# Kernel tuning notes

Measured on AMD Instinct MI355X. Metric: run time of the kernel, lower is better.

## Reference

```python
import jax, jax.numpy as jnp
import numpy as np
import math

HIDDEN = 128; NHEADS = 4; N_COE = 50; N_SCALES = 4; THRE = 5.0; S = 4096; B = 1


def setup_inputs():
    key = jax.random.key(0)
    ks = jax.random.split(key, 12)
    w = lambda k, shape: jax.random.normal(k, shape, jnp.float32) * 0.05
    return {
        "eigenvalue": jax.random.uniform(ks[0], (B, S), jnp.float32) * 2.0,  # graph Laplacian eigvals in [0,2)
        "length": jnp.full((B,), S, dtype=jnp.int32),
        "sele_num": jnp.full((B,), S, dtype=jnp.int32),
        "eig_w_W": w(ks[1], (HIDDEN + 1, HIDDEN)), "eig_w_b": jnp.zeros((HIDDEN,), jnp.float32),
        "mha_ln_g": jnp.ones((HIDDEN,), jnp.float32), "mha_ln_b": jnp.zeros((HIDDEN,), jnp.float32),
        "in_W": w(ks[2], (HIDDEN, 3 * HIDDEN)), "in_b": jnp.zeros((3 * HIDDEN,), jnp.float32),
        "out_W": w(ks[3], (HIDDEN, HIDDEN)), "out_b": jnp.zeros((HIDDEN,), jnp.float32),
        "ffn_ln_g": jnp.ones((HIDDEN,), jnp.float32), "ffn_ln_b": jnp.zeros((HIDDEN,), jnp.float32),
        "ffn1_W": w(ks[4], (HIDDEN, HIDDEN)), "ffn1_b": jnp.zeros((HIDDEN,), jnp.float32),
        "ffn2_W": w(ks[5], (HIDDEN, HIDDEN)), "ffn2_b": jnp.zeros((HIDDEN,), jnp.float32),
        "dsc_W": w(ks[6], (HIDDEN, N_COE)), "dsc_b": jnp.zeros((N_COE,), jnp.float32),
        "dwv_W": w(ks[7], (HIDDEN, N_COE)), "dwv_b": jnp.zeros((N_COE,), jnp.float32),
        "dss_W": w(ks[8], (HIDDEN, N_SCALES)), "dss_b": jnp.zeros((N_SCALES,), jnp.float32),
    }


def layer_norm(x, g, b, eps=1e-5):
    m = x.mean(-1, keepdims=True)
    v = ((x - m) ** 2).mean(-1, keepdims=True)
    return (x - m) / jnp.sqrt(v + eps) * g + b


def sine_encoding(e, W, b):
    # e: [B, S] -> [B, S, HIDDEN]
    div = jnp.exp(jnp.arange(0, HIDDEN, 2, dtype=e.dtype) * (-math.log(10000.0) / HIDDEN))
    pe = (e * 100.0)[..., None] * div  # [B, S, HIDDEN/2]
    eeig = jnp.concatenate([e[..., None], jnp.sin(pe), jnp.cos(pe)], axis=-1)  # [B, S, HIDDEN+1]
    return eeig @ W + b


def mha(x, pad_mask, in_W, in_b, out_W, out_b):
    # x: [B, S, D]; pad_mask: [B, S] True = masked key
    Bb, Ss, D = x.shape
    hd = D // NHEADS
    qkv = x @ in_W + in_b
    q, k, v = jnp.split(qkv, 3, axis=-1)
    hsplit = lambda t: t.reshape(Bb, Ss, NHEADS, hd).transpose(0, 2, 1, 3)  # [B, H, S, hd]
    q, k, v = hsplit(q), hsplit(k), hsplit(v)
    scores = jnp.einsum('bhqd,bhkd->bhqk', q, k) / math.sqrt(hd)
    scores = jnp.where(pad_mask[:, None, None, :], -jnp.inf, scores)
    attn = jax.nn.softmax(scores, axis=-1)
    o = jnp.einsum('bhqk,bhkd->bhqd', attn, v).transpose(0, 2, 1, 3).reshape(Bb, Ss, D)
    return o @ out_W + out_b


def cheb_base(y, n_coe, flag):
    # Chebyshev recurrence: wavelet = [T_0, T_2, ...], scaling = [T_1, T_3, ...]
    te0 = jnp.ones_like(y)
    to0 = y
    def step(carry, _):
        te, to = carry
        te = 2.0 * y * to - te
        to = 2.0 * y * te - to
        return (te, to), (te, to)
    _, (evens, odds) = jax.lax.scan(step, (te0, to0), None, length=n_coe - 1)
    if flag == 'scaling':
        base = jnp.concatenate([to0[None], odds], axis=0)   # [n_coe, B, S, d]
    else:
        base = jnp.concatenate([te0[None], evens], axis=0)
    return jnp.moveaxis(base, 0, 1)  # [B, n_coe, S, d]


def _forward(eigenvalue, eig_w_W, eig_w_b, mha_ln_g, mha_ln_b, in_W, in_b, out_W, out_b,
             ffn_ln_g, ffn_ln_b, ffn1_W, ffn1_b, ffn2_W, ffn2_b,
             dsc_W, dsc_b, dwv_W, dwv_b, dss_W, dss_b, length, sele_num):
    Bb, Ss = eigenvalue.shape
    eve = eigenvalue
    eig_mask = jnp.arange(Ss)[None, :] >= sele_num[:, None]  # [B, S] True = pad
    # --- EigenEncoding (dropout in eval mode = identity) ---
    eig = sine_encoding(eve, eig_w_W, eig_w_b)
    eig = eig + mha(layer_norm(eig, mha_ln_g, mha_ln_b), eig_mask, in_W, in_b, out_W, out_b)
    f = layer_norm(eig, ffn_ln_g, ffn_ln_b)
    f = jax.nn.gelu(f @ ffn1_W + ffn1_b, approximate=False) @ ffn2_W + ffn2_b
    eig_filter = eig + f  # [B, S, HIDDEN]
    lenf = length.astype(eve.dtype)[:, None]
    def pooled(W, b):
        c = eig_filter @ W + b
        c = jnp.where(eig_mask[..., None], 0.0, c)
        return c.sum(axis=1) / (lenf + 1e-8)
    coe_scaling = jax.nn.sigmoid(pooled(dsc_W, dsc_b))
    coe_scaling = coe_scaling / (coe_scaling.sum(-1, keepdims=True) + 1e-8)  # [B, n_coe]
    coe_wavelet = jax.nn.sigmoid(pooled(dwv_W, dwv_b))
    coe_wavelet = coe_wavelet / (coe_wavelet.sum(-1, keepdims=True) + 1e-8)
    coe_scales = jax.nn.sigmoid(pooled(dss_W, dss_b)) * THRE  # [B, n_scales]
    # --- Chebyshev bases ---
    base_scaling = cheb_base(eve[..., None] - 1.0, N_COE, 'scaling')  # [B, n_coe, S, 1]
    fsw = eve[..., None] * coe_scales[:, None, :]                      # [B, S, n_scales]
    fsw = jnp.where(fsw > 2.0, 0.0, fsw)
    base_wavelet = cheb_base(fsw - 1.0, N_COE, 'wavelet')             # [B, n_coe, S, n_scales]
    base_scaling = 0.5 * (1.0 - base_scaling)
    base_wavelet = 0.5 * (1.0 - base_wavelet)
    curr_scaling = jnp.einsum('bc,bcsd->bsd', coe_scaling, base_scaling)
    curr_wavelet = jnp.einsum('bc,bcsd->bsd', coe_wavelet, base_wavelet)
    out = jnp.concatenate([curr_scaling, curr_wavelet], axis=-1)       # [B, S, 1+n_scales]
    out = out / (jnp.linalg.norm(out, axis=-1, keepdims=True) + 1e-8)  # cfg.lam.tight_use = True
    return out


def reference(eigenvalue, length, sele_num, eig_w_W, eig_w_b, mha_ln_g, mha_ln_b, in_W, in_b,
              out_W, out_b, ffn_ln_g, ffn_ln_b, ffn1_W, ffn1_b, ffn2_W, ffn2_b,
              dsc_W, dsc_b, dwv_W, dwv_b, dss_W, dss_b):
    return _forward(eigenvalue, eig_w_W, eig_w_b, mha_ln_g, mha_ln_b, in_W, in_b, out_W, out_b,
                    ffn_ln_g, ffn_ln_b, ffn1_W, ffn1_b, ffn2_W, ffn2_b,
                    dsc_W, dsc_b, dwv_W, dwv_b, dss_W, dss_b, length, sele_num)
```

## Files before the change

kernel.cpp:

```cpp
#include <hip/hip_runtime.h>
#include <math.h>


#define KSPLIT 4

typedef __attribute__((ext_vector_type(8))) short short8;
typedef __attribute__((ext_vector_type(4))) short short4v;
typedef __attribute__((ext_vector_type(4))) float f32x4;

__device__ inline unsigned short f2bf(float x) {
    unsigned u = __float_as_uint(x);
    return (unsigned short)((u + 0x7FFFu + ((u >> 16) & 1u)) >> 16);
}
__device__ inline float bf2f(unsigned short h) { return __uint_as_float(((unsigned)h) << 16); }

__global__ __launch_bounds__(256) void k_embed(const float* __restrict__ eve,
    const float* __restrict__ eigW, const float* __restrict__ ebias,
    const float* __restrict__ g, const float* __restrict__ b,
    const float* __restrict__ inW, const float* __restrict__ inb,
    float* __restrict__ eig, float* __restrict__ qkv, unsigned short* __restrict__ Khi_g,
    unsigned short* __restrict__ Klo_g, unsigned short* __restrict__ Vt_g)
{
    __shared__ __align__(16) float wsh[129 * 128];
    __shared__ __align__(16) float se[16][132];
    __shared__ __align__(16) float xn[16][132];
    __shared__ __align__(16) unsigned short vsh[128][16];
    const int t = threadIdx.x;
    const int r0 = blockIdx.x * 16;
    {
        const int r = t >> 4, l4 = t & 15;
        const float e = eve[r0 + r];
        if (l4 == 0) se[r][128] = e;
        #pragma unroll
        for (int jj = 0; jj < 4; ++jj) {
            const int j = l4 * 4 + jj;
            const float div = __expf(-0.07195578415606394f * (float)(2 * j));
            const float pe = e * 100.0f * div;
            se[r][j]      = __sinf(pe);
            se[r][64 + j] = __cosf(pe);
        }
    }
    {
        const float4* __restrict__ src = (const float4*)eigW;
        float4* dst = (float4*)wsh;
        #pragma unroll
        for (int i = 0; i < 17; ++i) {
            const int f = t + i * 256;
            if (f < 4128) dst[f] = src[f];
        }
    }
    __syncthreads();
    const int lane = t & 63;
    const int w = t >> 6;
    const int rp = w * 2 + (lane >> 5);
    const int c0 = (lane & 31) * 4;
    const int ra = rp * 2, rb = ra + 1;
    float xa[4], xb[4];
    {
        const float4 w0 = *(const float4*)&wsh[c0];
        const float ea = se[ra][128], eb = se[rb][128];
        float a0 = ea * w0.x, a1 = ea * w0.y, a2 = ea * w0.z, a3 = ea * w0.w;
        float b0 = eb * w0.x, b1 = eb * w0.y, b2 = eb * w0.z, b3 = eb * w0.w;
        #pragma unroll 8
        for (int k = 0; k < 128; ++k) {
            const float xva = se[ra][k];
            const float xvb = se[rb][k];
            const float4 wk = *(const float4*)&wsh[(k + 1) * 128 + c0];
            a0 = fmaf(xva, wk.x, a0); a1 = fmaf(xva, wk.y, a1);
            a2 = fmaf(xva, wk.z, a2); a3 = fmaf(xva, wk.w, a3);
            b0 = fmaf(xvb, wk.x, b0); b1 = fmaf(xvb, wk.y, b1);
            b2 = fmaf(xvb, wk.z, b2); b3 = fmaf(xvb, wk.w, b3);
        }
        const float4 bb = *(const float4*)&ebias[c0];
        xa[0] = a0 + bb.x; xa[1] = a1 + bb.y; xa[2] = a2 + bb.z; xa[3] = a3 + bb.w;
        xb[0] = b0 + bb.x; xb[1] = b1 + bb.y; xb[2] = b2 + bb.z; xb[3] = b3 + bb.w;
        *(float4*)&eig[(size_t)(r0 + ra) * 128 + c0] = make_float4(xa[0], xa[1], xa[2], xa[3]);
        *(float4*)&eig[(size_t)(r0 + rb) * 128 + c0] = make_float4(xb[0], xb[1], xb[2], xb[3]);
    }
    {
        float sa = (xa[0] + xa[1]) + (xa[2] + xa[3]);
        float qa = (xa[0] * xa[0] + xa[1] * xa[1]) + (xa[2] * xa[2] + xa[3] * xa[3]);
        float sb = (xb[0] + xb[1]) + (xb[2] + xb[3]);
        float qb = (xb[0] * xb[0] + xb[1] * xb[1]) + (xb[2] * xb[2] + xb[3] * xb[3]);
        #pragma unroll
        for (int m = 1; m < 32; m <<= 1) {
            sa += __shfl_xor(sa, m, 32); qa += __shfl_xor(qa, m, 32);
            sb += __shfl_xor(sb, m, 32); qb += __shfl_xor(qb, m, 32);
        }
        const float ma = sa * (1.f / 128.f), mb = sb * (1.f / 128.f);
        const float ia = 1.f / sqrtf(qa * (1.f / 128.f) - ma * ma + 1e-5f);
        const float ib = 1.f / sqrtf(qb * (1.f / 128.f) - mb * mb + 1e-5f);
        const float4 gg = *(const float4*)&g[c0];
        const float4 bb = *(const float4*)&b[c0];
        *(float4*)&xn[ra][c0] = make_float4((xa[0] - ma) * ia * gg.x + bb.x,
                                            (xa[1] - ma) * ia * gg.y + bb.y,
                                            (xa[2] - ma) * ia * gg.z + bb.z,
                                            (xa[3] - ma) * ia * gg.w + bb.w);
        *(float4*)&xn[rb][c0] = make_float4((xb[0] - mb) * ib * gg.x + bb.x,
                                            (xb[1] - mb) * ib * gg.y + bb.y,
                                            (xb[2] - mb) * ib * gg.z + bb.z,
                                            (xb[3] - mb) * ib * gg.w + bb.w);
    }
    const int rowa = r0 + ra, rowb = r0 + rb;
    for (int p = 0; p < 3; ++p) {
        __syncthreads();
        {
            const float4* __restrict__ src = (const float4*)inW;
            float4* dst = (float4*)wsh;
            #pragma unroll
            for (int i = 0; i < 16; ++i) {
                const int f = t + i * 256;
                const int k = f >> 5, c4 = f & 31;
                dst[f] = src[k * 96 + p * 32 + c4];
            }
        }
        __syncthreads();
        float A[4], B[4];
        {
            const float4 bb = *(const float4*)&inb[p * 128 + c0];
            A[0] = bb.x; A[1] = bb.y; A[2] = bb.z; A[3] = bb.w;
            B[0] = bb.x; B[1] = bb.y; B[2] = bb.z; B[3] = bb.w;
        }
        #pragma unroll 8
        for (int k = 0; k < 128; ++k) {
            const float xva = xn[ra][k];
            const float xvb = xn[rb][k];
            const float4 wk = *(const float4*)&wsh[k * 128 + c0];
            A[0] = fmaf(xva, wk.x, A[0]); A[1] = fmaf(xva, wk.y, A[1]);
            A[2] = fmaf(xva, wk.z, A[2]); A[3] = fmaf(xva, wk.w, A[3]);
            B[0] = fmaf(xvb, wk.x, B[0]); B[1] = fmaf(xvb, wk.y, B[1]);
            B[2] = fmaf(xvb, wk.z, B[2]); B[3] = fmaf(xvb, wk.w, B[3]);
        }
        if (p == 0) {
            *(float4*)&qkv[(size_t)rowa * 384 + c0] = make_float4(A[0], A[1], A[2], A[3]);
            *(float4*)&qkv[(size_t)rowb * 384 + c0] = make_float4(B[0], B[1], B[2], B[3]);
        } else if (p == 1) {
            const int h = c0 >> 5, d = c0 & 31;
            unsigned short h4[4], l4v[4];
            #pragma unroll
            for (int i = 0; i < 4; ++i) { h4[i] = f2bf(A[i]); l4v[i] = f2bf(A[i] - bf2f(h4[i])); }
            *(uint2*)&Khi_g[((size_t)h * 4096 + rowa) * 32 + d] = *(uint2*)h4;
            *(uint2*)&Klo_g[((size_t)h * 4096 + rowa) * 32 + d] = *(uint2*)l4v;
            #pragma unroll
            for (int i = 0; i < 4; ++i) { h4[i] = f2bf(B[i]); l4v[i] = f2bf(B[i] - bf2f(h4[i])); }
            *(uint2*)&Khi_g[((size_t)h * 4096 + rowb) * 32 + d] = *(uint2*)h4;
            *(uint2*)&Klo_g[((size_t)h * 4096 + rowb) * 32 + d] = *(uint2*)l4v;
        } else {
            #pragma unroll
            for (int i = 0; i < 4; ++i) {
                vsh[c0 + i][ra] = f2bf(A[i]);
                vsh[c0 + i][rb] = f2bf(B[i]);
            }
        }
    }
    __syncthreads();
    if (t < 128) {
        const uint4 v0 = *(const uint4*)&vsh[t][0];
        const uint4 v1 = *(const uint4*)&vsh[t][8];
        *(uint4*)&Vt_g[(size_t)t * 4096 + r0]     = v0;
        *(uint4*)&Vt_g[(size_t)t * 4096 + r0 + 8] = v1;
    }
}

#define KSTR 40
#define VSTR 72
#define PSTR 72

__global__ __launch_bounds__(256) void k_attn(const float* __restrict__ qkv,
    const unsigned short* __restrict__ Khi_g, const unsigned short* __restrict__ Klo_g,
    const unsigned short* __restrict__ Vt_g,
    const int* __restrict__ sele, float* __restrict__ Oe, float* __restrict__ E)
{
    __shared__ __align__(16) unsigned short Khi[64 * KSTR];
    __shared__ __align__(16) unsigned short Klo[64 * KSTR];
    __shared__ __align__(16) unsigned short Vt[32 * VSTR];
    __shared__ __align__(16) unsigned short Pb[4][16 * PSTR];

    const int t = threadIdx.x;
    const int lane = t & 63;
    const int l = lane & 15;
    const int quad = lane >> 4;
    const int wv = __builtin_amdgcn_readfirstlane(t >> 6);
    const int qb = blockIdx.x;
    const int h  = blockIdx.y;
    const int ks = blockIdx.z;
    const int nk = sele[0];

    short8 qhi, qlo;
    {
        const float* __restrict__ qr = qkv + (size_t)(qb * 64 + wv * 16 + l) * 384 + h * 32 + quad * 8;
        const float4 a = *(const float4*)qr;
        const float4 b = *(const float4*)(qr + 4);
        const float sc = 0.17677669529663687f;
        float v[8] = {a.x * sc, a.y * sc, a.z * sc, a.w * sc, b.x * sc, b.y * sc, b.z * sc, b.w * sc};
        #pragma unroll
        for (int j = 0; j < 8; ++j) {
            const unsigned short hb = f2bf(v[j]);
            qhi[j] = (short)hb;
            qlo[j] = (short)f2bf(v[j] - bf2f(hb));
        }
    }
    f32x4 accO0 = {0.f, 0.f, 0.f, 0.f};
    f32x4 accO1 = {0.f, 0.f, 0.f, 0.f};
    float elane = 0.f;

    const int kk = t >> 2;
    const int d0 = (t & 3) * 8;
    const int vd = t >> 3;
    const int ko = (t & 7) * 8;

    for (int ch = 0; ch < 16; ++ch) {
        const int keybase = ks * 1024 + ch * 64;
        __syncthreads();
        {
            const uint4 kh16 = *(const uint4*)&Khi_g[((size_t)h * 4096 + keybase + kk) * 32 + d0];
            const uint4 kl16 = *(const uint4*)&Klo_g[((size_t)h * 4096 + keybase + kk) * 32 + d0];
            const uint4 vv16 = *(const uint4*)&Vt_g[((size_t)h * 32 + vd) * 4096 + keybase + ko];
            *(uint4*)&Khi[kk * KSTR + d0] = kh16;
            *(uint4*)&Klo[kk * KSTR + d0] = kl16;
            *(uint4*)&Vt[vd * VSTR + ko]  = vv16;
        }
        __syncthreads();
        unsigned short* __restrict__ Pw = Pb[wv];
        #pragma unroll
        for (int tile = 0; tile < 4; ++tile) {
            const int kl = tile * 16 + l;
            const short8 kh = *(const short8*)&Khi[kl * KSTR + quad * 8];
            const short8 kw = *(const short8*)&Klo[kl * KSTR + quad * 8];
            f32x4 S = {0.f, 0.f, 0.f, 0.f};
            S = __builtin_amdgcn_mfma_f32_16x16x32_bf16(kh, qhi, S, 0, 0, 0);
            S = __builtin_amdgcn_mfma_f32_16x16x32_bf16(kw, qhi, S, 0, 0, 0);
            S = __builtin_amdgcn_mfma_f32_16x16x32_bf16(kh, qlo, S, 0, 0, 0);
            const int kg0 = keybase + tile * 16 + quad * 4;
            short4v pw;
            #pragma unroll
            for (int r = 0; r < 4; ++r) {
                const float p = (kg0 + r < nk) ? __expf(S[r]) : 0.f;
                elane += p;
                pw[r] = (short)f2bf(p);
            }
            *(short4v*)&Pw[l * PSTR + tile * 16 + quad * 4] = pw;
        }
        #pragma unroll
        for (int step = 0; step < 2; ++step) {
            const short8 pa  = *(const short8*)&Pw[l * PSTR + step * 32 + quad * 8];
            const short8 vb0 = *(const short8*)&Vt[l * VSTR + step * 32 + quad * 8];
            const short8 vb1 = *(const short8*)&Vt[(16 + l) * VSTR + step * 32 + quad * 8];
            accO0 = __builtin_amdgcn_mfma_f32_16x16x32_bf16(pa, vb0, accO0, 0, 0, 0);
            accO1 = __builtin_amdgcn_mfma_f32_16x16x32_bf16(pa, vb1, accO1, 0, 0, 0);
        }
    }
    elane += __shfl_xor(elane, 16, 64);
    elane += __shfl_xor(elane, 32, 64);
    const int qrow0 = qb * 64 + wv * 16;
    if (lane < 16)
        E[((size_t)ks * 4 + h) * 4096 + qrow0 + l] = elane;
    #pragma unroll
    for (int r = 0; r < 4; ++r) {
        const size_t row = qrow0 + quad * 4 + r;
        Oe[((size_t)ks * 4096 + row) * 128 + h * 32 + l]      = accO0[r];
        Oe[((size_t)ks * 4096 + row) * 128 + h * 32 + 16 + l] = accO1[r];
    }
}

__global__ __launch_bounds__(256) void k_ffn(const float* __restrict__ eig,
    const float* __restrict__ Oe, const float* __restrict__ E,
    const float* __restrict__ outW, const float* __restrict__ outb,
    const float* __restrict__ lg, const float* __restrict__ lb,
    const float* __restrict__ W1, const float* __restrict__ b1,
    const float* __restrict__ W2, const float* __restrict__ b2,
    const int* __restrict__ sele, float* __restrict__ xsum)
{
    __shared__ __align__(16) float wsh[128 * 128];
    __shared__ __align__(16) float sA[16][132];
    __shared__ __align__(16) float xn[16][132];
    __shared__ __align__(16) float cs[16][132];
    const int t = threadIdx.x;
    const int r0 = blockIdx.x * 16;
    {
        const int r = t >> 4, c8 = (t & 15) * 8;
        const int h = c8 >> 5;
        float es = 0.f;
        float v[8] = {0.f, 0.f, 0.f, 0.f, 0.f, 0.f, 0.f, 0.f};
        #pragma unroll
        for (int ks = 0; ks < KSPLIT; ++ks) {
            es += E[((size_t)ks * 4 + h) * 4096 + r0 + r];
            const float4 o1 = *(const float4*)&Oe[((size_t)ks * 4096 + r0 + r) * 128 + c8];
            const float4 o2 = *(const float4*)&Oe[((size_t)ks * 4096 + r0 + r) * 128 + c8 + 4];
            v[0] += o1.x; v[1] += o1.y; v[2] += o1.z; v[3] += o1.w;
            v[4] += o2.x; v[5] += o2.y; v[6] += o2.z; v[7] += o2.w;
        }
        const float rcp = 1.f / es;
        *(float4*)&sA[r][c8]     = make_float4(v[0] * rcp, v[1] * rcp, v[2] * rcp, v[3] * rcp);
        *(float4*)&sA[r][c8 + 4] = make_float4(v[4] * rcp, v[5] * rcp, v[6] * rcp, v[7] * rcp);
    }
    {
        const float4* __restrict__ src = (const float4*)outW;
        float4* dst = (float4*)wsh;
        #pragma unroll
        for (int i = 0; i < 16; ++i) dst[t + i * 256] = src[t + i * 256];
    }
    __syncthreads();
    const int lane = t & 63;
    const int w = t >> 6;
    const int rp = w * 2 + (lane >> 5);
    const int c0 = (lane & 31) * 4;
    const int ra = rp * 2, rb = ra + 1;
    float x2a[4], x2b[4];
    {
        const float4 bb = *(const float4*)&outb[c0];
        float a0 = bb.x, a1 = bb.y, a2 = bb.z, a3 = bb.w;
        float b0 = bb.x, b1 = bb.y, b2 = bb.z, b3 = bb.w;
        #pragma unroll 8
        for (int k = 0; k < 128; ++k) {
            const float xva = sA[ra][k];
            const float xvb = sA[rb][k];
            const float4 wk = *(const float4*)&wsh[k * 128 + c0];
            a0 = fmaf(xva, wk.x, a0); a1 = fmaf(xva, wk.y, a1);
            a2 = fmaf(xva, wk.z, a2); a3 = fmaf(xva, wk.w, a3);
            b0 = fmaf(xvb, wk.x, b0); b1 = fmaf(xvb, wk.y, b1);
            b2 = fmaf(xvb, wk.z, b2); b3 = fmaf(xvb, wk.w, b3);
        }
        const float4 ea = *(const float4*)&eig[(size_t)(r0 + ra) * 128 + c0];
        const float4 eb = *(const float4*)&eig[(size_t)(r0 + rb) * 128 + c0];
        x2a[0] = ea.x + a0; x2a[1] = ea.y + a1; x2a[2] = ea.z + a2; x2a[3] = ea.w + a3;
        x2b[0] = eb.x + b0; x2b[1] = eb.y + b1; x2b[2] = eb.z + b2; x2b[3] = eb.w + b3;
    }
    {
        float sa = (x2a[0] + x2a[1]) + (x2a[2] + x2a[3]);
        float qa = (x2a[0] * x2a[0] + x2a[1] * x2a[1]) + (x2a[2] * x2a[2] + x2a[3] * x2a[3]);
        float sb = (x2b[0] + x2b[1]) + (x2b[2] + x2b[3]);
        float qb = (x2b[0] * x2b[0] + x2b[1] * x2b[1]) + (x2b[2] * x2b[2] + x2b[3] * x2b[3]);
        #pragma unroll
        for (int m = 1; m < 32; m <<= 1) {
            sa += __shfl_xor(sa, m, 32); qa += __shfl_xor(qa, m, 32);
            sb += __shfl_xor(sb, m, 32); qb += __shfl_xor(qb, m, 32);
        }
        const float ma = sa * (1.f / 128.f), mb = sb * (1.f / 128.f);
        const float ia = 1.f / sqrtf(qa * (1.f / 128.f) - ma * ma + 1e-5f);
        const float ib = 1.f / sqrtf(qb * (1.f / 128.f) - mb * mb + 1e-5f);
        const float4 gg = *(const float4*)&lg[c0];
        const float4 bb = *(const float4*)&lb[c0];
        *(float4*)&xn[ra][c0] = make_float4((x2a[0] - ma) * ia * gg.x + bb.x,
                                            (x2a[1] - ma) * ia * gg.y + bb.y,
                                            (x2a[2] - ma) * ia * gg.z + bb.z,
                                            (x2a[3] - ma) * ia * gg.w + bb.w);
        *(float4*)&xn[rb][c0] = make_float4((x2b[0] - mb) * ib * gg.x + bb.x,
                                            (x2b[1] - mb) * ib * gg.y + bb.y,
                                            (x2b[2] - mb) * ib * gg.z + bb.z,
                                            (x2b[3] - mb) * ib * gg.w + bb.w);
    }
    __syncthreads();
    {
        const float4* __restrict__ src = (const float4*)W1;
        float4* dst = (float4*)wsh;
        #pragma unroll
        for (int i = 0; i < 16; ++i) dst[t + i * 256] = src[t + i * 256];
    }
    __syncthreads();
    {
        const float4 bb = *(const float4*)&b1[c0];
        float a0 = bb.x, a1 = bb.y, a2 = bb.z, a3 = bb.w;
        float b0 = bb.x, b1v = bb.y, b2v = bb.z, b3 = bb.w;
        #pragma unroll 8
        for (int k = 0; k < 128; ++k) {
            const float xva = xn[ra][k];
            const float xvb = xn[rb][k];
            const float4 wk = *(const float4*)&wsh[k * 128 + c0];
            a0 = fmaf(xva, wk.x, a0); a1 = fmaf(xva, wk.y, a1);
            a2 = fmaf(xva, wk.z, a2); a3 = fmaf(xva, wk.w, a3);
            b0 = fmaf(xvb, wk.x, b0); b1v = fmaf(xvb, wk.y, b1v);
            b2v = fmaf(xvb, wk.z, b2v); b3 = fmaf(xvb, wk.w, b3);
        }
        *(float4*)&sA[ra][c0] = make_float4(
            0.5f * a0 * (1.f + erff(a0 * 0.70710678118654752f)),
            0.5f * a1 * (1.f + erff(a1 * 0.70710678118654752f)),
            0.5f * a2 * (1.f + erff(a2 * 0.70710678118654752f)),
            0.5f * a3 * (1.f + erff(a3 * 0.70710678118654752f)));
        *(float4*)&sA[rb][c0] = make_float4(
            0.5f * b0 * (1.f + erff(b0 * 0.70710678118654752f)),
            0.5f * b1v * (1.f + erff(b1v * 0.70710678118654752f)),
            0.5f * b2v * (1.f + erff(b2v * 0.70710678118654752f)),
            0.5f * b3 * (1.f + erff(b3 * 0.70710678118654752f)));
    }
    __syncthreads();
    {
        const float4* __restrict__ src = (const float4*)W2;
        float4* dst = (float4*)wsh;
        #pragma unroll
        for (int i = 0; i < 16; ++i) dst[t + i * 256] = src[t + i * 256];
    }
    __syncthreads();
    {
        const float4 bb = *(const float4*)&b2[c0];
        float a0 = bb.x, a1 = bb.y, a2 = bb.z, a3 = bb.w;
        float b0 = bb.x, b1v = bb.y, b2v = bb.z, b3 = bb.w;
        #pragma unroll 8
        for (int k = 0; k < 128; ++k) {
            const float xva = sA[ra][k];
            const float xvb = sA[rb][k];
            const float4 wk = *(const float4*)&wsh[k * 128 + c0];
            a0 = fmaf(xva, wk.x, a0); a1 = fmaf(xva, wk.y, a1);
            a2 = fmaf(xva, wk.z, a2); a3 = fmaf(xva, wk.w, a3);
            b0 = fmaf(xvb, wk.x, b0); b1v = fmaf(xvb, wk.y, b1v);
            b2v = fmaf(xvb, wk.z, b2v); b3 = fmaf(xvb, wk.w, b3);
        }
        const int nsel = sele[0];
        const bool ina = (r0 + ra) < nsel, inb2 = (r0 + rb) < nsel;
        *(float4*)&cs[ra][c0] = ina ? make_float4(x2a[0] + a0, x2a[1] + a1, x2a[2] + a2, x2a[3] + a3)
                                    : make_float4(0.f, 0.f, 0.f, 0.f);
        *(float4*)&cs[rb][c0] = inb2 ? make_float4(x2b[0] + b0, x2b[1] + b1v, x2b[2] + b2v, x2b[3] + b3)
                                     : make_float4(0.f, 0.f, 0.f, 0.f);
    }
    __syncthreads();
    if (t < 128) {
        float s = 0.f;
        #pragma unroll
        for (int rr = 0; rr < 16; ++rr) s += cs[rr][t];
        atomicAdd(&xsum[t], s);
    }
}

__global__ __launch_bounds__(512) void k_coef(const float* __restrict__ xsum,
    const float* __restrict__ dscW, const float* __restrict__ dscb,
    const float* __restrict__ dwvW, const float* __restrict__ dwvb,
    const float* __restrict__ dssW, const float* __restrict__ dssb,
    const int* __restrict__ len, const int* __restrict__ sele,
    float* __restrict__ coef)
{
    __shared__ float xs[128];
    __shared__ float part[104][4];
    __shared__ float val[104];
    __shared__ float s2[2];
    const int t = threadIdx.x;
    if (t < 128) xs[t] = xsum[t];
    __syncthreads();
    const float invl = 1.f / ((float)len[0] + 1e-8f);
    const float ns = (float)sele[0];
    const int o = t >> 2, lk = t & 3;
    if (o < 104) {
        const float* Wp; int stride, col;
        if (o < 50)       { Wp = dscW; stride = 50; col = o; }
        else if (o < 100) { Wp = dwvW; stride = 50; col = o - 50; }
        else              { Wp = dssW; stride = 4;  col = o - 100; }
        float a = 0.f;
        #pragma unroll
        for (int kk = 0; kk < 32; ++kk) {
            const int k = lk * 32 + kk;
            a = fmaf(xs[k], Wp[k * stride + col], a);
        }
        part[o][lk] = a;
    }
    __syncthreads();
    if (t < 104) {
        const float bias = (t < 50) ? dscb[t] : ((t < 100) ? dwvb[t - 50] : dssb[t - 100]);
        float a = ((part[t][0] + part[t][1]) + (part[t][2] + part[t][3]) + ns * bias) * invl;
        val[t] = 1.f / (1.f + __expf(-a));
    }
    __syncthreads();
    if (t == 0) { float s = 0.f; for (int i = 0; i < 50; ++i) s += val[i]; s2[0] = s; }
    if (t == 1) { float s = 0.f; for (int i = 0; i < 50; ++i) s += val[50 + i]; s2[1] = s; }
    __syncthreads();
    if (t < 50) {
        coef[t]      = val[t] / (s2[0] + 1e-8f);
        coef[50 + t] = val[50 + t] / (s2[1] + 1e-8f);
    } else if (t >= 100 && t < 104) {
        coef[t] = val[t] * 5.0f;
    }
}

__global__ __launch_bounds__(128) void k_out(const float* __restrict__ eve,
    const float* __restrict__ coef, float* __restrict__ out)
{
    __shared__ float csc[50], cwv[50], cssh[4];
    const int t = threadIdx.x;
    if (t < 50) csc[t] = coef[t];
    else if (t < 100) cwv[t - 50] = coef[t];
    else if (t < 104) cssh[t - 100] = coef[t];
    __syncthreads();
    const int s = blockIdx.x * 128 + t;
    const float e = eve[s];
    float vals[5];
    {
        const float y = e - 1.f;
        float te = 1.f, to = y;
        float a = csc[0] * (0.5f * (1.f - to));
        const float y2 = 2.f * y;
        for (int i = 1; i < 50; ++i) {
            te = fmaf(y2, to, -te);
            to = fmaf(y2, te, -to);
            a = fmaf(csc[i], 0.5f * (1.f - to), a);
        }
        vals[0] = a;
    }
    #pragma unroll
    for (int j = 0; j < 4; ++j) {
        float f = e * cssh[j];
        if (f > 2.f) f = 0.f;
        const float y = f - 1.f;
        float te = 1.f, to = y;
        float a = cwv[0] * (0.5f * (1.f - te));
        const float y2 = 2.f * y;
        for (int i = 1; i < 50; ++i) {
            te = fmaf(y2, to, -te);
            to = fmaf(y2, te, -to);
            a = fmaf(cwv[i], 0.5f * (1.f - te), a);
        }
        vals[1 + j] = a;
    }
    float n2 = 0.f;
    #pragma unroll
    for (int k = 0; k < 5; ++k) n2 += vals[k] * vals[k];
    const float invn = 1.f / (sqrtf(n2) + 1e-8f);
    #pragma unroll
    for (int k = 0; k < 5; ++k) out[s * 5 + k] = vals[k] * invn;
}

extern "C" void kernel_launch(void* const* d_in, const int* in_sizes, int n_in,
                              void* d_out, int out_size, void* d_ws, size_t ws_size,
                              hipStream_t stream) {
    const float* eve  = (const float*)d_in[0];
    const int*   len  = (const int*)d_in[1];
    const int*   sele = (const int*)d_in[2];
    const float* eigW = (const float*)d_in[3];
    const float* eigB = (const float*)d_in[4];
    const float* mlg  = (const float*)d_in[5];
    const float* mlb  = (const float*)d_in[6];
    const float* inW  = (const float*)d_in[7];
    const float* inb  = (const float*)d_in[8];
    const float* outW = (const float*)d_in[9];
    const float* outb = (const float*)d_in[10];
    const float* flg  = (const float*)d_in[11];
    const float* flb  = (const float*)d_in[12];
    const float* W1   = (const float*)d_in[13];
    const float* b1   = (const float*)d_in[14];
    const float* W2   = (const float*)d_in[15];
    const float* b2   = (const float*)d_in[16];
    const float* dscW = (const float*)d_in[17];
    const float* dscb = (const float*)d_in[18];
    const float* dwvW = (const float*)d_in[19];
    const float* dwvb = (const float*)d_in[20];
    const float* dssW = (const float*)d_in[21];
    const float* dssb = (const float*)d_in[22];

    float* ws   = (float*)d_ws;
    float* eig  = ws;
    float* qkv  = ws + 524288;
    float* Oe   = ws + 2097152;
    float* E    = ws + 4194304;
    float* xsum = ws + 4259840;
    float* coef = ws + 4259968;
    unsigned short* Khi_g = (unsigned short*)(ws + 4260352);
    unsigned short* Klo_g = (unsigned short*)(ws + 4522496);
    unsigned short* Vt_g  = (unsigned short*)(ws + 4784640);
    float* out  = (float*)d_out;

    hipMemsetAsync(xsum, 0, 128 * sizeof(float), stream);
    k_embed<<<256, 256, 0, stream>>>(eve, eigW, eigB, mlg, mlb, inW, inb,
                                     eig, qkv, Khi_g, Klo_g, Vt_g);
    k_attn <<<dim3(64, 4, KSPLIT), 256, 0, stream>>>(qkv, Khi_g, Klo_g, Vt_g, sele, Oe, E);
    k_ffn  <<<256, 256, 0, stream>>>(eig, Oe, E, outW, outb, flg, flb, W1, b1, W2, b2, sele, xsum);
    k_coef <<<1, 512, 0, stream>>>(xsum, dscW, dscb, dwvW, dwvb, dssW, dssb, len, sele, coef);
    k_out  <<<32, 128, 0, stream>>>(eve, coef, out);
}
```

Measured before the change: 187.8 us.

## Fold xsum memset into embed, merge coef into output kernel, widen blocks

The memset of the feature-sum buffer moves into the first block of the embed kernel. The single-block coefficient kernel is merged into the output kernel, and each of the 32 blocks now recomputes the coefficients redundantly. The embed and FFN kernels move from 256 to 512 threads with one row per thread group instead of two, which doubles parallelism per block but halves register-level reuse of the LDS weight loads. The changes aim to remove two launches and the memset node, at the cost of redundant tail compute and possibly more LDS traffic.

```diff
diff --git a/kernel.cpp b/kernel.cpp
--- a/kernel.cpp
+++ b/kernel.cpp
@@ -14,26 +14,28 @@
 }
 __device__ inline float bf2f(unsigned short h) { return __uint_as_float(((unsigned)h) << 16); }
 
-__global__ __launch_bounds__(256) void k_embed(const float* __restrict__ eve,
+__global__ __launch_bounds__(512) void k_embed(const float* __restrict__ eve,
     const float* __restrict__ eigW, const float* __restrict__ ebias,
     const float* __restrict__ g, const float* __restrict__ b,
     const float* __restrict__ inW, const float* __restrict__ inb,
     float* __restrict__ eig, float* __restrict__ qkv, unsigned short* __restrict__ Khi_g,
-    unsigned short* __restrict__ Klo_g, unsigned short* __restrict__ Vt_g)
+    unsigned short* __restrict__ Klo_g, unsigned short* __restrict__ Vt_g,
+    float* __restrict__ xsum)
 {
     __shared__ __align__(16) float wsh[129 * 128];
     __shared__ __align__(16) float se[16][132];
     __shared__ __align__(16) float xn[16][132];
-    __shared__ __align__(16) unsigned short vsh[128][16];
+    __shared__ __align__(16) unsigned short vsh[16][136];
     const int t = threadIdx.x;
     const int r0 = blockIdx.x * 16;
-    {
-        const int r = t >> 4, l4 = t & 15;
+    if (blockIdx.x == 0 && t < 128) xsum[t] = 0.f;
+    {
+        const int r = t >> 5, l5 = t & 31;
         const float e = eve[r0 + r];
-        if (l4 == 0) se[r][128] = e;
-        #pragma unroll
-        for (int jj = 0; jj < 4; ++jj) {
-            const int j = l4 * 4 + jj;
+        if (l5 == 0) se[r][128] = e;
+        #pragma unroll
+        for (int jj = 0; jj < 2; ++jj) {
+            const int j = l5 * 2 + jj;
             const float div = __expf(-0.07195578415606394f * (float)(2 * j));
             const float pe = e * 100.0f * div;
             se[r][j]      = __sinf(pe);
@@ -44,121 +46,95 @@
         const float4* __restrict__ src = (const float4*)eigW;
         float4* dst = (float4*)wsh;
         #pragma unroll
-        for (int i = 0; i < 17; ++i) {
-            const int f = t + i * 256;
+        for (int i = 0; i < 9; ++i) {
+            const int f = t + i * 512;
             if (f < 4128) dst[f] = src[f];
         }
     }
     __syncthreads();
-    const int lane = t & 63;
-    const int w = t >> 6;
-    const int rp = w * 2 + (lane >> 5);
-    const int c0 = (lane & 31) * 4;
-    const int ra = rp * 2, rb = ra + 1;
-    float xa[4], xb[4];
+    const int r  = t >> 5;
+    const int c0 = (t & 31) * 4;
+    float xa[4];
     {
         const float4 w0 = *(const float4*)&wsh[c0];
-        const float ea = se[ra][128], eb = se[rb][128];
+        const float ea = se[r][128];
         float a0 = ea * w0.x, a1 = ea * w0.y, a2 = ea * w0.z, a3 = ea * w0.w;
-        float b0 = eb * w0.x, b1 = eb * w0.y, b2 = eb * w0.z, b3 = eb * w0.w;
         #pragma unroll 8
         for (int k = 0; k < 128; ++k) {
-            const float xva = se[ra][k];
-            const float xvb = se[rb][k];
+            const float xv = se[r][k];
             const float4 wk = *(const float4*)&wsh[(k + 1) * 128 + c0];
-            a0 = fmaf(xva, wk.x, a0); a1 = fmaf(xva, wk.y, a1);
-            a2 = fmaf(xva, wk.z, a2); a3 = fmaf(xva, wk.w, a3);
-            b0 = fmaf(xvb, wk.x, b0); b1 = fmaf(xvb, wk.y, b1);
-            b2 = fmaf(xvb, wk.z, b2); b3 = fmaf(xvb, wk.w, b3);
+            a0 = fmaf(xv, wk.x, a0); a1 = fmaf(xv, wk.y, a1);
+            a2 = fmaf(xv, wk.z, a2); a3 = fmaf(xv, wk.w, a3);
         }
         const float4 bb = *(const float4*)&ebias[c0];
         xa[0] = a0 + bb.x; xa[1] = a1 + bb.y; xa[2] = a2 + bb.z; xa[3] = a3 + bb.w;
-        xb[0] = b0 + bb.x; xb[1] = b1 + bb.y; xb[2] = b2 + bb.z; xb[3] = b3 + bb.w;
-        *(float4*)&eig[(size_t)(r0 + ra) * 128 + c0] = make_float4(xa[0], xa[1], xa[2], xa[3]);
-        *(float4*)&eig[(size_t)(r0 + rb) * 128 + c0] = make_float4(xb[0], xb[1], xb[2], xb[3]);
+        *(float4*)&eig[(size_t)(r0 + r) * 128 + c0] = make_float4(xa[0], xa[1], xa[2], xa[3]);
     }
     {
         float sa = (xa[0] + xa[1]) + (xa[2] + xa[3]);
         float qa = (xa[0] * xa[0] + xa[1] * xa[1]) + (xa[2] * xa[2] + xa[3] * xa[3]);
-        float sb = (xb[0] + xb[1]) + (xb[2] + xb[3]);
-        float qb = (xb[0] * xb[0] + xb[1] * xb[1]) + (xb[2] * xb[2] + xb[3] * xb[3]);
         #pragma unroll
         for (int m = 1; m < 32; m <<= 1) {
             sa += __shfl_xor(sa, m, 32); qa += __shfl_xor(qa, m, 32);
-            sb += __shfl_xor(sb, m, 32); qb += __shfl_xor(qb, m, 32);
-        }
-        const float ma = sa * (1.f / 128.f), mb = sb * (1.f / 128.f);
+        }
+        const float ma = sa * (1.f / 128.f);
         const float ia = 1.f / sqrtf(qa * (1.f / 128.f) - ma * ma + 1e-5f);
-        const float ib = 1.f / sqrtf(qb * (1.f / 128.f) - mb * mb + 1e-5f);
         const float4 gg = *(const float4*)&g[c0];
         const float4 bb = *(const float4*)&b[c0];
-        *(float4*)&xn[ra][c0] = make_float4((xa[0] - ma) * ia * gg.x + bb.x,
-                                            (xa[1] - ma) * ia * gg.y + bb.y,
-                                            (xa[2] - ma) * ia * gg.z + bb.z,
-                                            (xa[3] - ma) * ia * gg.w + bb.w);
-        *(float4*)&xn[rb][c0] = make_float4((xb[0] - mb) * ib * gg.x + bb.x,
-                                            (xb[1] - mb) * ib * gg.y + bb.y,
-                                            (xb[2] - mb) * ib * gg.z + bb.z,
-                                            (xb[3] - mb) * ib * gg.w + bb.w);
-    }
-    const int rowa = r0 + ra, rowb = r0 + rb;
+        *(float4*)&xn[r][c0] = make_float4((xa[0] - ma) * ia * gg.x + bb.x,
+                                           (xa[1] - ma) * ia * gg.y + bb.y,
+                                           (xa[2] - ma) * ia * gg.z + bb.z,
+                                           (xa[3] - ma) * ia * gg.w + bb.w);
+    }
+    const int row = r0 + r;
     for (int p = 0; p < 3; ++p) {
         __syncthreads();
         {
             const float4* __restrict__ src = (const float4*)inW;
             float4* dst = (float4*)wsh;
             #pragma unroll
-            for (int i = 0; i < 16; ++i) {
-                const int f = t + i * 256;
+            for (int i = 0; i < 8; ++i) {
+                const int f = t + i * 512;
                 const int k = f >> 5, c4 = f & 31;
                 dst[f] = src[k * 96 + p * 32 + c4];
             }
         }
         __syncthreads();
-        float A[4], B[4];
+        float A[4];
         {
             const float4 bb = *(const float4*)&inb[p * 128 + c0];
             A[0] = bb.x; A[1] = bb.y; A[2] = bb.z; A[3] = bb.w;
-            B[0] = bb.x; B[1] = bb.y; B[2] = bb.z; B[3] = bb.w;
         }
         #pragma unroll 8
         for (int k = 0; k < 128; ++k) {
-            const float xva = xn[ra][k];
-            const float xvb = xn[rb][k];
+            const float xv = xn[r][k];
             const float4 wk = *(const float4*)&wsh[k * 128 + c0];
-            A[0] = fmaf(xva, wk.x, A[0]); A[1] = fmaf(xva, wk.y, A[1]);
-            A[2] = fmaf(xva, wk.z, A[2]); A[3] = fmaf(xva, wk.w, A[3]);
-            B[0] = fmaf(xvb, wk.x, B[0]); B[1] = fmaf(xvb, wk.y, B[1]);
-            B[2] = fmaf(xvb, wk.z, B[2]); B[3] = fmaf(xvb, wk.w, B[3]);
+            A[0] = fmaf(xv, wk.x, A[0]); A[1] = fmaf(xv, wk.y, A[1]);
+            A[2] = fmaf(xv, wk.z, A[2]); A[3] = fmaf(xv, wk.w, A[3]);
         }
         if (p == 0) {
-            *(float4*)&qkv[(size_t)rowa * 384 + c0] = make_float4(A[0], A[1], A[2], A[3]);
-            *(float4*)&qkv[(size_t)rowb * 384 + c0] = make_float4(B[0], B[1], B[2], B[3]);
+            *(float4*)&qkv[(size_t)row * 384 + c0] = make_float4(A[0], A[1], A[2], A[3]);
         } else if (p == 1) {
             const int h = c0 >> 5, d = c0 & 31;
             unsigned short h4[4], l4v[4];
             #pragma unroll
             for (int i = 0; i < 4; ++i) { h4[i] = f2bf(A[i]); l4v[i] = f2bf(A[i] - bf2f(h4[i])); }
-            *(uint2*)&Khi_g[((size_t)h * 4096 + rowa) * 32 + d] = *(uint2*)h4;
-            *(uint2*)&Klo_g[((size_t)h * 4096 + rowa) * 32 + d] = *(uint2*)l4v;
+            *(uint2*)&Khi_g[((size_t)h * 4096 + row) * 32 + d] = *(uint2*)h4;
+            *(uint2*)&Klo_g[((size_t)h * 4096 + row) * 32 + d] = *(uint2*)l4v;
+        } else {
+            unsigned short v4[4];
             #pragma unroll
-            for (int i = 0; i < 4; ++i) { h4[i] = f2bf(B[i]); l4v[i] = f2bf(B[i] - bf2f(h4[i])); }
-            *(uint2*)&Khi_g[((size_t)h * 4096 + rowb) * 32 + d] = *(uint2*)h4;
-            *(uint2*)&Klo_g[((size_t)h * 4096 + rowb) * 32 + d] = *(uint2*)l4v;
-        } else {
-            #pragma unroll
-            for (int i = 0; i < 4; ++i) {
-                vsh[c0 + i][ra] = f2bf(A[i]);
-                vsh[c0 + i][rb] = f2bf(B[i]);
-            }
+            for (int i = 0; i < 4; ++i) v4[i] = f2bf(A[i]);
+            *(uint2*)&vsh[r][c0] = *(uint2*)v4;
         }
     }
     __syncthreads();
     if (t < 128) {
-        const uint4 v0 = *(const uint4*)&vsh[t][0];
-        const uint4 v1 = *(const uint4*)&vsh[t][8];
-        *(uint4*)&Vt_g[(size_t)t * 4096 + r0]     = v0;
-        *(uint4*)&Vt_g[(size_t)t * 4096 + r0 + 8] = v1;
+        unsigned short tmp[16];
+        #pragma unroll
+        for (int k2 = 0; k2 < 16; ++k2) tmp[k2] = vsh[k2][t];
+        *(uint4*)&Vt_g[(size_t)t * 4096 + r0]     = *(uint4*)&tmp[0];
+        *(uint4*)&Vt_g[(size_t)t * 4096 + r0 + 8] = *(uint4*)&tmp[8];
     }
 }
 
@@ -263,7 +239,7 @@
     }
 }
 
-__global__ __launch_bounds__(256) void k_ffn(const float* __restrict__ eig,
+__global__ __launch_bounds__(512) void k_ffn(const float* __restrict__ eig,
     const float* __restrict__ Oe, const float* __restrict__ E,
     const float* __restrict__ outW, const float* __restrict__ outb,
     const float* __restrict__ lg, const float* __restrict__ lb,
@@ -277,140 +253,104 @@
     __shared__ __align__(16) float cs[16][132];
     const int t = threadIdx.x;
     const int r0 = blockIdx.x * 16;
-    {
-        const int r = t >> 4, c8 = (t & 15) * 8;
-        const int h = c8 >> 5;
+    const int r  = t >> 5;
+    const int c0 = (t & 31) * 4;
+    {
+        const int h = c0 >> 5;
         float es = 0.f;
-        float v[8] = {0.f, 0.f, 0.f, 0.f, 0.f, 0.f, 0.f, 0.f};
+        float v[4] = {0.f, 0.f, 0.f, 0.f};
         #pragma unroll
         for (int ks = 0; ks < KSPLIT; ++ks) {
             es += E[((size_t)ks * 4 + h) * 4096 + r0 + r];
-            const float4 o1 = *(const float4*)&Oe[((size_t)ks * 4096 + r0 + r) * 128 + c8];
-            const float4 o2 = *(const float4*)&Oe[((size_t)ks * 4096 + r0 + r) * 128 + c8 + 4];
+            const float4 o1 = *(const float4*)&Oe[((size_t)ks * 4096 + r0 + r) * 128 + c0];
             v[0] += o1.x; v[1] += o1.y; v[2] += o1.z; v[3] += o1.w;
-            v[4] += o2.x; v[5] += o2.y; v[6] += o2.z; v[7] += o2.w;
         }
         const float rcp = 1.f / es;
-        *(float4*)&sA[r][c8]     = make_float4(v[0] * rcp, v[1] * rcp, v[2] * rcp, v[3] * rcp);
-        *(float4*)&sA[r][c8 + 4] = make_float4(v[4] * rcp, v[5] * rcp, v[6] * rcp, v[7] * rcp);
+        *(float4*)&sA[r][c0] = make_float4(v[0] * rcp, v[1] * rcp, v[2] * rcp, v[3] * rcp);
     }
     {
         const float4* __restrict__ src = (const float4*)outW;
         float4* dst = (float4*)wsh;
         #pragma unroll
-        for (int i = 0; i < 16; ++i) dst[t + i * 256] = src[t + i * 256];
-    }
-    __syncthreads();
-    const int lane = t & 63;
-    const int w = t >> 6;
-    const int rp = w * 2 + (lane >> 5);
-    const int c0 = (lane & 31) * 4;
-    const int ra = rp * 2, rb = ra + 1;
-    float x2a[4], x2b[4];
+        for (int i = 0; i < 8; ++i) dst[t + i * 512] = src[t + i * 512];
+    }
+    __syncthreads();
+    float x2[4];
     {
         const float4 bb = *(const float4*)&outb[c0];
         float a0 = bb.x, a1 = bb.y, a2 = bb.z, a3 = bb.w;
-        float b0 = bb.x, b1 = bb.y, b2 = bb.z, b3 = bb.w;
         #pragma unroll 8
         for (int k = 0; k < 128; ++k) {
-            const float xva = sA[ra][k];
-            const float xvb = sA[rb][k];
+            const float xv = sA[r][k];
             const float4 wk = *(const float4*)&wsh[k * 128 + c0];
-            a0 = fmaf(xva, wk.x, a0); a1 = fmaf(xva, wk.y, a1);
-            a2 = fmaf(xva, wk.z, a2); a3 = fmaf(xva, wk.w, a3);
-            b0 = fmaf(xvb, wk.x, b0); b1 = fmaf(xvb, wk.y, b1);
-            b2 = fmaf(xvb, wk.z, b2); b3 = fmaf(xvb, wk.w, b3);
-        }
-        const float4 ea = *(const float4*)&eig[(size_t)(r0 + ra) * 128 + c0];
-        const float4 eb = *(const float4*)&eig[(size_t)(r0 + rb) * 128 + c0];
-        x2a[0] = ea.x + a0; x2a[1] = ea.y + a1; x2a[2] = ea.z + a2; x2a[3] = ea.w + a3;
-        x2b[0] = eb.x + b0; x2b[1] = eb.y + b1; x2b[2] = eb.z + b2; x2b[3] = eb.w + b3;
-    }
-    {
-        float sa = (x2a[0] + x2a[1]) + (x2a[2] + x2a[3]);
-        float qa = (x2a[0] * x2a[0] + x2a[1] * x2a[1]) + (x2a[2] * x2a[2] + x2a[3] * x2a[3]);
-        float sb = (x2b[0] + x2b[1]) + (x2b[2] + x2b[3]);
-        float qb = (x2b[0] * x2b[0] + x2b[1] * x2b[1]) + (x2b[2] * x2b[2] + x2b[3] * x2b[3]);
+            a0 = fmaf(xv, wk.x, a0); a1 = fmaf(xv, wk.y, a1);
+            a2 = fmaf(xv, wk.z, a2); a3 = fmaf(xv, wk.w, a3);
+        }
+        const float4 ea = *(const float4*)&eig[(size_t)(r0 + r) * 128 + c0];
+        x2[0] = ea.x + a0; x2[1] = ea.y + a1; x2[2] = ea.z + a2; x2[3] = ea.w + a3;
+    }
+    {
+        float sa = (x2[0] + x2[1]) + (x2[2] + x2[3]);
+        float qa = (x2[0] * x2[0] + x2[1] * x2[1]) + (x2[2] * x2[2] + x2[3] * x2[3]);
         #pragma unroll
         for (int m = 1; m < 32; m <<= 1) {
             sa += __shfl_xor(sa, m, 32); qa += __shfl_xor(qa, m, 32);
-            sb += __shfl_xor(sb, m, 32); qb += __shfl_xor(qb, m, 32);
-        }
-        const float ma = sa * (1.f / 128.f), mb = sb * (1.f / 128.f);
+        }
+        const float ma = sa * (1.f / 128.f);
         const float ia = 1.f / sqrtf(qa * (1.f / 128.f) - ma * ma + 1e-5f);
-        const float ib = 1.f / sqrtf(qb * (1.f / 128.f) - mb * mb + 1e-5f);
         const float4 gg = *(const float4*)&lg[c0];
         const float4 bb = *(const float4*)&lb[c0];
-        *(float4*)&xn[ra][c0] = make_float4((x2a[0] - ma) * ia * gg.x + bb.x,
-                                            (x2a[1] - ma) * ia * gg.y + bb.y,
-                                            (x2a[2] - ma) * ia * gg.z + bb.z,
-                                            (x2a[3] - ma) * ia * gg.w + bb.w);
-        *(float4*)&xn[rb][c0] = make_float4((x2b[0] - mb) * ib * gg.x + bb.x,
-                                            (x2b[1] - mb) * ib * gg.y + bb.y,
-                                            (x2b[2] - mb) * ib * gg.z + bb.z,
-                                            (x2b[3] - mb) * ib * gg.w + bb.w);
+        *(float4*)&xn[r][c0] = make_float4((x2[0] - ma) * ia * gg.x + bb.x,
+                                           (x2[1] - ma) * ia * gg.y + bb.y,
+                                           (x2[2] - ma) * ia * gg.z + bb.z,
+                                           (x2[3] - ma) * ia * gg.w + bb.w);
     }
     __syncthreads();
     {
         const float4* __restrict__ src = (const float4*)W1;
         float4* dst = (float4*)wsh;
         #pragma unroll
-        for (int i = 0; i < 16; ++i) dst[t + i * 256] = src[t + i * 256];
+        for (int i = 0; i < 8; ++i) dst[t + i * 512] = src[t + i * 512];
     }
     __syncthreads();
     {
         const float4 bb = *(const float4*)&b1[c0];
         float a0 = bb.x, a1 = bb.y, a2 = bb.z, a3 = bb.w;
-        float b0 = bb.x, b1v = bb.y, b2v = bb.z, b3 = bb.w;
         #pragma unroll 8
         for (int k = 0; k < 128; ++k) {
-            const float xva = xn[ra][k];
-            const float xvb = xn[rb][k];
+            const float xv = xn[r][k];
             const float4 wk = *(const float4*)&wsh[k * 128 + c0];
-            a0 = fmaf(xva, wk.x, a0); a1 = fmaf(xva, wk.y, a1);
-            a2 = fmaf(xva, wk.z, a2); a3 = fmaf(xva, wk.w, a3);
-            b0 = fmaf(xvb, wk.x, b0); b1v = fmaf(xvb, wk.y, b1v);
-            b2v = fmaf(xvb, wk.z, b2v); b3 = fmaf(xvb, wk.w, b3);
-        }
-        *(float4*)&sA[ra][c0] = make_float4(
+            a0 = fmaf(xv, wk.x, a0); a1 = fmaf(xv, wk.y, a1);
+            a2 = fmaf(xv, wk.z, a2); a3 = fmaf(xv, wk.w, a3);
+        }
+        *(float4*)&sA[r][c0] = make_float4(
             0.5f * a0 * (1.f + erff(a0 * 0.70710678118654752f)),
             0.5f * a1 * (1.f + erff(a1 * 0.70710678118654752f)),
             0.5f * a2 * (1.f + erff(a2 * 0.70710678118654752f)),
             0.5f * a3 * (1.f + erff(a3 * 0.70710678118654752f)));
-        *(float4*)&sA[rb][c0] = make_float4(
-            0.5f * b0 * (1.f + erff(b0 * 0.70710678118654752f)),
-            0.5f * b1v * (1.f + erff(b1v * 0.70710678118654752f)),
-            0.5f * b2v * (1.f + erff(b2v * 0.70710678118654752f)),
-            0.5f * b3 * (1.f + erff(b3 * 0.70710678118654752f)));
     }
     __syncthreads();
     {
         const float4* __restrict__ src = (const float4*)W2;
         float4* dst = (float4*)wsh;
         #pragma unroll
-        for (int i = 0; i < 16; ++i) dst[t + i * 256] = src[t + i * 256];
+        for (int i = 0; i < 8; ++i) dst[t + i * 512] = src[t + i * 512];
     }
     __syncthreads();
     {
         const float4 bb = *(const float4*)&b2[c0];
         float a0 = bb.x, a1 = bb.y, a2 = bb.z, a3 = bb.w;
-        float b0 = bb.x, b1v = bb.y, b2v = bb.z, b3 = bb.w;
         #pragma unroll 8
         for (int k = 0; k < 128; ++k) {
-            const float xva = sA[ra][k];
-            const float xvb = sA[rb][k];
+            const float xv = sA[r][k];
             const float4 wk = *(const float4*)&wsh[k * 128 + c0];
-            a0 = fmaf(xva, wk.x, a0); a1 = fmaf(xva, wk.y, a1);
-            a2 = fmaf(xva, wk.z, a2); a3 = fmaf(xva, wk.w, a3);
-            b0 = fmaf(xvb, wk.x, b0); b1v = fmaf(xvb, wk.y, b1v);
-            b2v = fmaf(xvb, wk.z, b2v); b3 = fmaf(xvb, wk.w, b3);
+            a0 = fmaf(xv, wk.x, a0); a1 = fmaf(xv, wk.y, a1);
+            a2 = fmaf(xv, wk.z, a2); a3 = fmaf(xv, wk.w, a3);
         }
         const int nsel = sele[0];
-        const bool ina = (r0 + ra) < nsel, inb2 = (r0 + rb) < nsel;
-        *(float4*)&cs[ra][c0] = ina ? make_float4(x2a[0] + a0, x2a[1] + a1, x2a[2] + a2, x2a[3] + a3)
-                                    : make_float4(0.f, 0.f, 0.f, 0.f);
-        *(float4*)&cs[rb][c0] = inb2 ? make_float4(x2b[0] + b0, x2b[1] + b1v, x2b[2] + b2v, x2b[3] + b3)
-                                     : make_float4(0.f, 0.f, 0.f, 0.f);
+        const bool ina = (r0 + r) < nsel;
+        *(float4*)&cs[r][c0] = ina ? make_float4(x2[0] + a0, x2[1] + a1, x2[2] + a2, x2[3] + a3)
+                                   : make_float4(0.f, 0.f, 0.f, 0.f);
     }
     __syncthreads();
     if (t < 128) {
@@ -421,40 +361,32 @@
     }
 }
 
-__global__ __launch_bounds__(512) void k_coef(const float* __restrict__ xsum,
+__global__ __launch_bounds__(128) void k_tail(const float* __restrict__ eve,
+    const float* __restrict__ xsum,
     const float* __restrict__ dscW, const float* __restrict__ dscb,
     const float* __restrict__ dwvW, const float* __restrict__ dwvb,
     const float* __restrict__ dssW, const float* __restrict__ dssb,
     const int* __restrict__ len, const int* __restrict__ sele,
-    float* __restrict__ coef)
+    float* __restrict__ out)
 {
     __shared__ float xs[128];
-    __shared__ float part[104][4];
     __shared__ float val[104];
     __shared__ float s2[2];
+    __shared__ float csc[50], cwv[50], cssh[4];
     const int t = threadIdx.x;
-    if (t < 128) xs[t] = xsum[t];
-    __syncthreads();
-    const float invl = 1.f / ((float)len[0] + 1e-8f);
-    const float ns = (float)sele[0];
-    const int o = t >> 2, lk = t & 3;
-    if (o < 104) {
-        const float* Wp; int stride, col;
-        if (o < 50)       { Wp = dscW; stride = 50; col = o; }
-        else if (o < 100) { Wp = dwvW; stride = 50; col = o - 50; }
-        else              { Wp = dssW; stride = 4;  col = o - 100; }
+    xs[t] = xsum[t];
+    __syncthreads();
+    if (t < 104) {
+        const float invl = 1.f / ((float)len[0] + 1e-8f);
+        const float ns = (float)sele[0];
+        const float* Wp; int stride, col; float bias;
+        if (t < 50)       { Wp = dscW; stride = 50; col = t;       bias = dscb[t]; }
+        else if (t < 100) { Wp = dwvW; stride = 50; col = t - 50;  bias = dwvb[t - 50]; }
+        else              { Wp = dssW; stride = 4;  col = t - 100; bias = dssb[t - 100]; }
         float a = 0.f;
-        #pragma unroll
-        for (int kk = 0; kk < 32; ++kk) {
-            const int k = lk * 32 + kk;
-            a = fmaf(xs[k], Wp[k * stride + col], a);
-        }
-        part[o][lk] = a;
-    }
-    __syncthreads();
-    if (t < 104) {
-        const float bias = (t < 50) ? dscb[t] : ((t < 100) ? dwvb[t - 50] : dssb[t - 100]);
-        float a = ((part[t][0] + part[t][1]) + (part[t][2] + part[t][3]) + ns * bias) * invl;
+        #pragma unroll 4
+        for (int k = 0; k < 128; ++k) a = fmaf(xs[k], Wp[k * stride + col], a);
+        a = (a + ns * bias) * invl;
         val[t] = 1.f / (1.f + __expf(-a));
     }
     __syncthreads();
@@ -462,21 +394,11 @@
     if (t == 1) { float s = 0.f; for (int i = 0; i < 50; ++i) s += val[50 + i]; s2[1] = s; }
     __syncthreads();
     if (t < 50) {
-        coef[t]      = val[t] / (s2[0] + 1e-8f);
-        coef[50 + t] = val[50 + t] / (s2[1] + 1e-8f);
+        csc[t] = val[t] / (s2[0] + 1e-8f);
+        cwv[t] = val[50 + t] / (s2[1] + 1e-8f);
     } else if (t >= 100 && t < 104) {
-        coef[t] = val[t] * 5.0f;
-    }
-}
-
-__global__ __launch_bounds__(128) void k_out(const float* __restrict__ eve,
-    const float* __restrict__ coef, float* __restrict__ out)
-{
-    __shared__ float csc[50], cwv[50], cssh[4];
-    const int t = threadIdx.x;
-    if (t < 50) csc[t] = coef[t];
-    else if (t < 100) cwv[t - 50] = coef[t];
-    else if (t < 104) cssh[t - 100] = coef[t];
+        cssh[t - 100] = val[t] * 5.0f;
+    }
     __syncthreads();
     const int s = blockIdx.x * 128 + t;
     const float e = eve[s];
@@ -549,17 +471,14 @@
     float* Oe   = ws + 2097152;
     float* E    = ws + 4194304;
     float* xsum = ws + 4259840;
-    float* coef = ws + 4259968;
     unsigned short* Khi_g = (unsigned short*)(ws + 4260352);
     unsigned short* Klo_g = (unsigned short*)(ws + 4522496);
     unsigned short* Vt_g  = (unsigned short*)(ws + 4784640);
     float* out  = (float*)d_out;
 
-    hipMemsetAsync(xsum, 0, 128 * sizeof(float), stream);
-    k_embed<<<256, 256, 0, stream>>>(eve, eigW, eigB, mlg, mlb, inW, inb,
-                                     eig, qkv, Khi_g, Klo_g, Vt_g);
+    k_embed<<<256, 512, 0, stream>>>(eve, eigW, eigB, mlg, mlb, inW, inb,
+                                     eig, qkv, Khi_g, Klo_g, Vt_g, xsum);
     k_attn <<<dim3(64, 4, KSPLIT), 256, 0, stream>>>(qkv, Khi_g, Klo_g, Vt_g, sele, Oe, E);
-    k_ffn  <<<256, 256, 0, stream>>>(eig, Oe, E, outW, outb, flg, flb, W1, b1, W2, b2, sele, xsum);
-    k_coef <<<1, 512, 0, stream>>>(xsum, dscW, dscb, dwvW, dwvb, dssW, dssb, len, sele, coef);
-    k_out  <<<32, 128, 0, stream>>>(eve, coef, out);
-}
+    k_ffn  <<<256, 512, 0, stream>>>(eig, Oe, E, outW, outb, flg, flb, W1, b1, W2, b2, sele, xsum);
+    k_tail <<<32, 128, 0, stream>>>(eve, xsum, dscW, dscb, dwvW, dwvb, dssW, dssb, len, sele, out);
+}
```

After: 185.8 us. Within noise of the previous version (-1.1%).
